# Kernel optimization log

Hardware: AMD Instinct MI355X
Metric: run time of the kernel (lower is better)

Reference implementation:

```python
import jax, jax.numpy as jnp
import numpy as np

NUM_EDGE = 5
NUM_CHANNELS = 2
NUM_NODES = 2048
W_IN = 256
W_OUT = 128
NUM_CLASS = 16
NUM_LAYERS = 2


def gtconv(A, w):
    """Softmax-weighted mix of edge-type adjacencies.
    A: [E, N, N], w: [E, C] -> [C, N, N].
    Equivalent to concatenating COO edge lists scaled by filter[j, i] and
    summing duplicates (what the scipy round-trip does implicitly)."""
    f = jax.nn.softmax(w, axis=0)  # softmax over edge types (dim=0)
    return jnp.einsum('enm,ec->cnm', A, f)


def degree_normalize(H):
    """GTN.normalization: deg = scatter_add over col, value *= deg[col]^-1 (col scaling).
    H: [C, N, N]; deg over rows (axis=1) gives per-column in-degree."""
    deg = H.sum(axis=1)  # [C, N]
    dinv = jnp.where(deg > 0, 1.0 / jnp.where(deg > 0, deg, 1.0), 0.0)
    return H * dinv[:, None, :]


def setup_inputs() -> dict:
    key = jax.random.key(0)
    ks = jax.random.split(key, 8)
    A = jax.random.uniform(ks[0], (NUM_EDGE, NUM_NODES, NUM_NODES), dtype=jnp.float32)
    h = jax.random.normal(ks[1], (NUM_NODES, W_IN), dtype=jnp.float32)
    # GTConv weights: init std=0.01 as in reset_parameters
    w1 = jax.random.normal(ks[2], (NUM_EDGE, NUM_CHANNELS), dtype=jnp.float32) * 0.01
    w2 = jax.random.normal(ks[3], (NUM_EDGE, NUM_CHANNELS), dtype=jnp.float32) * 0.01
    w_layers = jax.random.normal(ks[4], (NUM_LAYERS - 1, NUM_EDGE, NUM_CHANNELS), dtype=jnp.float32) * 0.01
    gcn_w = jax.random.normal(ks[5], (W_IN, W_OUT), dtype=jnp.float32) * (1.0 / np.sqrt(W_IN))
    gcn_b = jnp.zeros((W_OUT,), dtype=jnp.float32)
    lin1_w = jax.random.normal(ks[6], (W_OUT * NUM_CHANNELS, W_OUT), dtype=jnp.float32) * (1.0 / np.sqrt(W_OUT * NUM_CHANNELS))
    lin1_b = jnp.zeros((W_OUT,), dtype=jnp.float32)
    lin2_w = jax.random.normal(ks[7], (W_OUT, NUM_CLASS), dtype=jnp.float32) * (1.0 / np.sqrt(W_OUT))
    lin2_b = jnp.zeros((NUM_CLASS,), dtype=jnp.float32)
    return {"A": A, "h": h, "w1": w1, "w2": w2, "w_layers": w_layers,
            "gcn_w": gcn_w, "gcn_b": gcn_b, "lin1_w": lin1_w, "lin1_b": lin1_b,
            "lin2_w": lin2_w, "lin2_b": lin2_b}


def reference(A, h, w1, w2, w_layers, gcn_w, gcn_b, lin1_w, lin1_b, lin2_w, lin2_b):
    # Layer 0 (first=True): H[c] = conv1(A)[c] @ conv2(A)[c], then degree norm.
    H = jnp.einsum('cnk,ckm->cnm', gtconv(A, w1), gtconv(A, w2))
    H = degree_normalize(H)
    # Layers 1..L-1 (first=False): H[c] = H[c] @ conv(A)[c], then degree norm.
    for i in range(w_layers.shape[0]):
        B = gtconv(A, w_layers[i])
        H = jnp.einsum('cnk,ckm->cnm', H, B)
        H = degree_normalize(H)
    # Shared GCN per channel (DGL GraphConv, norm='both'): weight first (w_in > w_out),
    # src out-degree^-1/2 scaling, aggregate along edges src->dst, dst in-degree^-1/2.
    hw = h @ gcn_w                                   # [N, w_out]
    dout = jnp.clip(H.sum(axis=2), 1.0, None) ** -0.5  # [C, N] src norm
    din = jnp.clip(H.sum(axis=1), 1.0, None) ** -0.5   # [C, N] dst norm
    agg = jnp.einsum('cnm,cnd->cmd', H, dout[:, :, None] * hw[None])  # dst m gathers from src n
    X = jax.nn.relu(agg * din[:, :, None] + gcn_b)   # [C, N, w_out]
    # Concatenate channels along feature dim (channel-major, matching th.cat order)
    X = jnp.transpose(X, (1, 0, 2)).reshape(H.shape[1], -1)  # [N, C*w_out]
    X = jax.nn.relu(X @ lin1_w + lin1_b)
    return X @ lin2_w + lin2_b
```

## Files before the change

### kernel.cpp

```cpp
#include <hip/hip_runtime.h>

typedef unsigned short u16;
typedef __attribute__((ext_vector_type(4))) float f32x4;
typedef __attribute__((ext_vector_type(8))) __bf16 bf16x8;
typedef __attribute__((ext_vector_type(8))) unsigned short us8;

#define NN (2048ull*2048ull)

__device__ __forceinline__ u16 f2b(float x){
  union { float f; unsigned u; } v; v.f = x;
  unsigned r = v.u + 0x7FFFu + ((v.u >> 16) & 1u);
  return (u16)(r >> 16);
}
__device__ __forceinline__ float b2f(u16 x){
  union { unsigned u; float f; } v; v.u = ((unsigned)x) << 16; return v.f;
}

__global__ __launch_bounds__(256)
void k_mix(const float* __restrict__ A,
           const float* __restrict__ w1, const float* __restrict__ w2,
           const float* __restrict__ wl,
           u16* __restrict__ A1, u16* __restrict__ A2T, u16* __restrict__ BT,
           float* __restrict__ zbuf){
  __shared__ u16 lt[4][64][72];
  const int t = threadIdx.x;
  if (blockIdx.x == 0 && blockIdx.y == 0){
    #pragma unroll
    for (int i=0;i<48;i++) zbuf[i*256 + t] = 0.f;
  }
  const int mq = t & 15, nr = t >> 4;
  const int n0 = blockIdx.y * 64, m0 = blockIdx.x * 64;
  float f[3][2][5];
  #pragma unroll
  for (int s=0;s<3;s++){
    const float* w = (s==0) ? w1 : (s==1) ? w2 : wl;
    #pragma unroll
    for (int c=0;c<2;c++){
      float m = -1e30f;
      #pragma unroll
      for (int e=0;e<5;e++) m = fmaxf(m, w[e*2+c]);
      float sum = 0.f;
      #pragma unroll
      for (int e=0;e<5;e++){ f[s][c][e] = __expf(w[e*2+c]-m); sum += f[s][c][e]; }
      float inv = 1.f/sum;
      #pragma unroll
      for (int e=0;e<5;e++) f[s][c][e] *= inv;
    }
  }

  #pragma unroll
  for (int rr=0; rr<4; ++rr){
    const int nl = nr*4 + rr;
    const size_t off = (size_t)(n0+nl)*2048 + m0 + mq*4;
    float4 a0 = *(const float4*)&A[off];
    float4 a1 = *(const float4*)&A[NN + off];
    float4 a2 = *(const float4*)&A[2*NN + off];
    float4 a3 = *(const float4*)&A[3*NN + off];
    float4 a4 = *(const float4*)&A[4*NN + off];
    float ax[4][5] = {{a0.x,a1.x,a2.x,a3.x,a4.x},
                      {a0.y,a1.y,a2.y,a3.y,a4.y},
                      {a0.z,a1.z,a2.z,a3.z,a4.z},
                      {a0.w,a1.w,a2.w,a3.w,a4.w}};
    #pragma unroll
    for (int c=0;c<2;c++){
      ushort4 o1, o2, o3;
      #pragma unroll
      for (int j=0;j<4;j++){
        float s1=0.f,s2=0.f,s3=0.f;
        #pragma unroll
        for (int e=0;e<5;e++){
          s1 += ax[j][e]*f[0][c][e];
          s2 += ax[j][e]*f[1][c][e];
          s3 += ax[j][e]*f[2][c][e];
        }
        ((u16*)&o1)[j] = f2b(s1);
        ((u16*)&o2)[j] = f2b(s2);
        ((u16*)&o3)[j] = f2b(s3);
      }
      *(ushort4*)&A1[(size_t)c*NN + off] = o1;
      *(ushort4*)&lt[c][nl][mq*4] = o2;
      *(ushort4*)&lt[2+c][nl][mq*4] = o3;
    }
  }
  __syncthreads();
  const int nq = t & 15, mr = t >> 4;
  #pragma unroll
  for (int s=0;s<4;s++){
    u16* __restrict__ dst = (s<2) ? A2T : BT;
    const int c = s & 1;
    #pragma unroll
    for (int rr=0;rr<4;rr++){
      const int ml = mr*4 + rr;
      ushort4 o;
      o.x = lt[s][nq*4+0][ml];
      o.y = lt[s][nq*4+1][ml];
      o.z = lt[s][nq*4+2][ml];
      o.w = lt[s][nq*4+3][ml];
      *(ushort4*)&dst[(size_t)c*NN + (size_t)(m0+ml)*2048 + n0 + nq*4] = o;
    }
  }
}

template<bool TRANS>
__global__ __launch_bounds__(512, 2)
void k_gemm_big(const u16* __restrict__ A, const u16* __restrict__ Bt,
                u16* __restrict__ C, float* __restrict__ deg){
  __shared__ u16 lA[2][256*64];
  __shared__ u16 lB[2][128*64];
  const int tid = threadIdx.x;
  const int bm = blockIdx.x, bn = blockIdx.y, cc = blockIdx.z;
  const u16* __restrict__ Ab = A + (size_t)cc*NN + (size_t)(bm*256)*2048;
  const u16* __restrict__ Bb = Bt + (size_t)cc*NN + (size_t)(bn*128)*2048;
  const int wid = tid >> 6, lane = tid & 63;
  const int wr = wid >> 1, wc = wid & 1;
  const int fl = lane & 15, fkg = lane >> 4;
  const int srow = tid >> 3;
  const int scol_sw = ((tid & 7) ^ (srow & 7)) << 3;
  const int csw0 = (((0*4 + fkg) ^ (fl & 7)) << 3);
  const int csw1 = (((1*4 + fkg) ^ (fl & 7)) << 3);

  f32x4 acc[4][4];
  const f32x4 zero = {0.f,0.f,0.f,0.f};
  #pragma unroll
  for (int i=0;i<4;i++)
    #pragma unroll
    for (int jj=0;jj<4;jj++) acc[i][jj] = zero;

  auto stage = [&](int buf, int k0){
    #pragma unroll
    for (int i=0;i<4;++i)
      __builtin_amdgcn_global_load_lds(
        (const __attribute__((address_space(1))) void*)(Ab + (size_t)(i*64 + srow)*2048 + k0 + scol_sw),
        (__attribute__((address_space(3))) void*)(&lA[buf][(i*512 + (wid<<6))<<3]), 16, 0, 0);
    #pragma unroll
    for (int i=0;i<2;++i)
      __builtin_amdgcn_global_load_lds(
        (const __attribute__((address_space(1))) void*)(Bb + (size_t)(i*64 + srow)*2048 + k0 + scol_sw),
        (__attribute__((address_space(3))) void*)(&lB[buf][(i*512 + (wid<<6))<<3]), 16, 0, 0);
  };

  auto compute = [&](const u16* __restrict__ ca, const u16* __restrict__ cb){
    bf16x8 af[2][4], bfr[2][4];
    #pragma unroll
    for (int mi=0;mi<4;mi++){
      af[0][mi] = *reinterpret_cast<const bf16x8*>(&ca[(wr*64 + mi*16 + fl)*64 + csw0]);
      af[1][mi] = *reinterpret_cast<const bf16x8*>(&ca[(wr*64 + mi*16 + fl)*64 + csw1]);
    }
    #pragma unroll
    for (int ni=0;ni<4;ni++){
      bfr[0][ni] = *reinterpret_cast<const bf16x8*>(&cb[(wc*64 + ni*16 + fl)*64 + csw0]);
      bfr[1][ni] = *reinterpret_cast<const bf16x8*>(&cb[(wc*64 + ni*16 + fl)*64 + csw1]);
    }
    __builtin_amdgcn_sched_barrier(0);
    __builtin_amdgcn_s_setprio(1);
    #pragma unroll
    for (int ks=0; ks<2; ++ks)
      #pragma unroll
      for (int mi=0;mi<4;mi++)
        #pragma unroll
        for (int ni=0;ni<4;ni++)
          acc[mi][ni] = __builtin_amdgcn_mfma_f32_16x16x32_bf16(af[ks][mi], bfr[ks][ni], acc[mi][ni], 0, 0, 0);
    __builtin_amdgcn_s_setprio(0);
    __builtin_amdgcn_sched_barrier(0);
  };

  stage(0, 0);
  stage(1, 64);
  int cur = 0;
  #pragma unroll 2
  for (int t = 0; t < 30; ++t){
    asm volatile("s_waitcnt vmcnt(6)" ::: "memory");
    __builtin_amdgcn_sched_barrier(0);
    __builtin_amdgcn_s_barrier();
    __builtin_amdgcn_sched_barrier(0);
    compute(&lA[cur][0], &lB[cur][0]);
    __builtin_amdgcn_s_barrier();
    __builtin_amdgcn_sched_barrier(0);
    stage(cur, (t+2)*64);
    cur ^= 1;
  }
  asm volatile("s_waitcnt vmcnt(6)" ::: "memory");
  __builtin_amdgcn_sched_barrier(0);
  __builtin_amdgcn_s_barrier();
  __builtin_amdgcn_sched_barrier(0);
  compute(&lA[cur][0], &lB[cur][0]);
  cur ^= 1;
  asm volatile("s_waitcnt vmcnt(0)" ::: "memory");
  __builtin_amdgcn_sched_barrier(0);
  __builtin_amdgcn_s_barrier();
  __builtin_amdgcn_sched_barrier(0);
  compute(&lA[cur][0], &lB[cur][0]);

  #pragma unroll
  for (int ni=0; ni<4; ++ni){
    float cs = 0.f;
    #pragma unroll
    for (int mi=0;mi<4;mi++)
      #pragma unroll
      for (int r=0;r<4;r++) cs += acc[mi][ni][r];
    cs += __shfl_xor(cs, 16);
    cs += __shfl_xor(cs, 32);
    if (lane < 16)
      atomicAdd(&deg[cc*2048 + bn*128 + wc*64 + ni*16 + fl], cs);
  }
  const int rbase = fkg << 2;
  if (!TRANS){
    u16* __restrict__ Cb = C + (size_t)cc*NN + (size_t)(bm*256 + wr*64)*2048 + bn*128 + wc*64;
    #pragma unroll
    for (int mi=0;mi<4;mi++)
      #pragma unroll
      for (int ni=0;ni<4;ni++)
        #pragma unroll
        for (int r=0;r<4;r++)
          Cb[(size_t)(mi*16 + rbase + r)*2048 + ni*16 + fl] = f2b(acc[mi][ni][r]);
  } else {
    u16* __restrict__ Cb = C + (size_t)cc*NN + (size_t)(bn*128 + wc*64)*2048 + bm*256 + wr*64;
    #pragma unroll
    for (int ni=0;ni<4;ni++)
      #pragma unroll
      for (int mi=0;mi<4;mi++){
        ushort4 o;
        o.x = f2b(acc[mi][ni][0]); o.y = f2b(acc[mi][ni][1]);
        o.z = f2b(acc[mi][ni][2]); o.w = f2b(acc[mi][ni][3]);
        *(ushort4*)&Cb[(size_t)(ni*16 + fl)*2048 + mi*16 + rbase] = o;
      }
  }
}

__global__ void k_btscale(u16* __restrict__ BT, const float* __restrict__ deg){
  size_t idx = (size_t)blockIdx.x*256 + threadIdx.x;
  int c  = (int)(idx >> 19);
  int k8 = ((int)(idx & 255)) * 8;
  us8 v = ((const us8*)BT)[idx];
  #pragma unroll
  for (int j=0;j<8;j++){
    float d = deg[c*2048 + k8 + j];
    float di = d > 0.f ? 1.f/d : 0.f;
    v[j] = f2b(b2f(v[j]) * di);
  }
  ((us8*)BT)[idx] = v;
}

__global__ __launch_bounds__(256)
void k_wcolsum(const u16* __restrict__ HT, const float* __restrict__ deg2,
               float* __restrict__ rowsum){
  __shared__ float sdi[128];
  const int t = threadIdx.x;
  const int n = blockIdx.x * 256 + t;
  const int m0 = blockIdx.y * 128;
  const int c = blockIdx.z;
  if (t < 128){
    float d = deg2[c*2048 + m0 + t];
    sdi[t] = d > 0.f ? 1.f/d : 0.f;
  }
  __syncthreads();
  const u16* __restrict__ p = HT + (size_t)c*NN + (size_t)m0*2048 + n;
  float s = 0.f;
  #pragma unroll 4
  for (int m=0;m<128;m++)
    s += b2f(p[(size_t)m*2048]) * sdi[m];
  atomicAdd(&rowsum[c*2048 + n], s);
}

__global__ __launch_bounds__(256)
void k_hw(const float* __restrict__ h, const float* __restrict__ W, float* __restrict__ hw){
  __shared__ float lh[16][256];
  int t = threadIdx.x;
  int n0 = blockIdx.x * 16;
  for (int idx = t; idx < 16*256; idx += 256)
    lh[idx >> 8][idx & 255] = h[(size_t)(n0 + (idx>>8))*256 + (idx&255)];
  __syncthreads();
  int d = t & 127, half = t >> 7;
  float acc[8];
  #pragma unroll
  for (int nn=0;nn<8;nn++) acc[nn] = 0.f;
  for (int k=0;k<256;k++){
    float wv = W[(size_t)k*128 + d];
    #pragma unroll
    for (int nn=0;nn<8;nn++) acc[nn] += lh[half*8+nn][k]*wv;
  }
  #pragma unroll
  for (int nn=0;nn<8;nn++) hw[(size_t)(n0 + half*8 + nn)*128 + d] = acc[nn];
}

__global__ void k_pt(const float* __restrict__ hw, const float* __restrict__ rowsum,
                     u16* __restrict__ PT){
  int t = threadIdx.x;
  int n = blockIdx.x * 64 + (t & 63);
  int c = blockIdx.y;
  float dv = rsqrtf(fmaxf(rowsum[c*2048 + n], 1.0f));
  for (int d = t >> 6; d < 128; d += 4)
    PT[((size_t)c*128 + d)*2048 + n] = f2b(dv * hw[(size_t)n*128 + d]);
}

__global__ __launch_bounds__(256, 2)
void k_gemm3(const u16* __restrict__ A, const u16* __restrict__ Bt, float* __restrict__ Cp){
  __shared__ u16 lA[128*64];
  __shared__ u16 lB[128*64];
  const int tid = threadIdx.x;
  const int bm = blockIdx.x, bk = blockIdx.y, cc = blockIdx.z;
  const u16* __restrict__ Ab = A + (size_t)cc*NN + (size_t)(bm*128)*2048 + bk*256;
  const u16* __restrict__ Bb = Bt + (size_t)cc*(128*2048) + bk*256;
  float* __restrict__ Cb = Cp + ((size_t)bk*2 + cc)*2048*128 + (size_t)(bm*128)*128;
  const int wid = tid >> 6, lane = tid & 63;
  const int wr = wid >> 1, wc = wid & 1;
  const int fl = lane & 15, fk = (lane >> 4) << 3;
  const int srow = (wid << 3) + (lane >> 3);
  const int scol = (lane & 7) << 3;

  f32x4 acc[4][4];
  const f32x4 zero = {0.f,0.f,0.f,0.f};
  #pragma unroll
  for (int i=0;i<4;i++)
    #pragma unroll
    for (int jj=0;jj<4;jj++) acc[i][jj] = zero;

  for (int k0 = 0; k0 < 256; k0 += 64){
    #pragma unroll
    for (int it = 0; it < 4; ++it){
      int r = it*32 + srow;
      __builtin_amdgcn_global_load_lds(
        (const __attribute__((address_space(1))) void*)(Ab + (size_t)r*2048 + k0 + scol),
        (__attribute__((address_space(3))) void*)(&lA[(it*32 + (wid<<3))*64]), 16, 0, 0);
      __builtin_amdgcn_global_load_lds(
        (const __attribute__((address_space(1))) void*)(Bb + (size_t)r*2048 + k0 + scol),
        (__attribute__((address_space(3))) void*)(&lB[(it*32 + (wid<<3))*64]), 16, 0, 0);
    }
    __syncthreads();
    #pragma unroll
    for (int ks = 0; ks < 2; ++ks){
      bf16x8 af[4], bfr[4];
      #pragma unroll
      for (int mi=0;mi<4;mi++)
        af[mi] = *reinterpret_cast<const bf16x8*>(&lA[(wr*64 + mi*16 + fl)*64 + ks*32 + fk]);
      #pragma unroll
      for (int ni=0;ni<4;ni++)
        bfr[ni] = *reinterpret_cast<const bf16x8*>(&lB[(wc*64 + ni*16 + fl)*64 + ks*32 + fk]);
      #pragma unroll
      for (int mi=0;mi<4;mi++)
        #pragma unroll
        for (int ni=0;ni<4;ni++)
          acc[mi][ni] = __builtin_amdgcn_mfma_f32_16x16x32_bf16(af[mi], bfr[ni], acc[mi][ni], 0, 0, 0);
    }
    __syncthreads();
  }
  const int rbase = (lane >> 4) << 2;
  #pragma unroll
  for (int mi=0;mi<4;mi++)
    #pragma unroll
    for (int ni=0;ni<4;ni++)
      #pragma unroll
      for (int r=0;r<4;r++)
        Cb[(size_t)(wr*64 + mi*16 + rbase + r)*128 + wc*64 + ni*16 + fl] = acc[mi][ni][r];
}

__global__ __launch_bounds__(256)
void k_head(const float* __restrict__ aggp, const float* __restrict__ deg2,
            const float* __restrict__ gb,
            const float* __restrict__ W1, const float* __restrict__ b1,
            const float* __restrict__ W2, const float* __restrict__ b2,
            float* __restrict__ out){
  __shared__ float lx[16][256];
  __shared__ float lt[16][132];
  int t = threadIdx.x;
  int n0 = blockIdx.x * 16;
  for (int idx = t; idx < 1024; idx += 256){
    int row = idx >> 6;
    int q = idx & 63;
    int c = q >> 5, d4 = (q & 31) * 4;
    float dg = deg2[c*2048 + n0 + row];
    float di = dg > 0.f ? 1.f/dg : 0.f;
    float4 s = {0.f,0.f,0.f,0.f};
    #pragma unroll
    for (int p=0;p<8;p++){
      const float4 v = *(const float4*)&aggp[(((size_t)p*2 + c)*2048 + n0 + row)*128 + d4];
      s.x += v.x; s.y += v.y; s.z += v.z; s.w += v.w;
    }
    const float4 bv = *(const float4*)&gb[d4];
    s.x = fmaxf(s.x*di + bv.x, 0.f); s.y = fmaxf(s.y*di + bv.y, 0.f);
    s.z = fmaxf(s.z*di + bv.z, 0.f); s.w = fmaxf(s.w*di + bv.w, 0.f);
    *(float4*)&lx[row][c*128 + d4] = s;
  }
  __syncthreads();
  int d = t & 127, half = t >> 7;
  float acc[8];
  #pragma unroll
  for (int nn=0;nn<8;nn++) acc[nn] = 0.f;
  for (int k=0;k<256;k++){
    float wv = W1[(size_t)k*128 + d];
    #pragma unroll
    for (int nn=0;nn<8;nn++) acc[nn] += lx[half*8+nn][k]*wv;
  }
  float bb = b1[d];
  #pragma unroll
  for (int nn=0;nn<8;nn++){
    float v = acc[nn] + bb;
    lt[half*8+nn][d] = v > 0.f ? v : 0.f;
  }
  __syncthreads();
  {
    int row = t >> 4, q = t & 15;
    float s = b2[q];
    for (int dd=0; dd<128; dd++) s += lt[row][dd] * W2[(size_t)dd*16 + q];
    out[(size_t)(n0+row)*16 + q] = s;
  }
}

extern "C" void kernel_launch(void* const* d_in, const int* in_sizes, int n_in,
                              void* d_out, int out_size, void* d_ws, size_t ws_size,
                              hipStream_t stream){
  const float* A   = (const float*)d_in[0];
  const float* h   = (const float*)d_in[1];
  const float* w1  = (const float*)d_in[2];
  const float* w2  = (const float*)d_in[3];
  const float* wl  = (const float*)d_in[4];
  const float* gw  = (const float*)d_in[5];
  const float* gb  = (const float*)d_in[6];
  const float* l1w = (const float*)d_in[7];
  const float* l1b = (const float*)d_in[8];
  const float* l2w = (const float*)d_in[9];
  const float* l2b = (const float*)d_in[10];
  float* out = (float*)d_out;
  char* ws = (char*)d_ws;

  const size_t SZ = 2*NN*2;
  u16*  A1   = (u16*)(ws);
  u16*  A2T  = (u16*)(ws + 1*SZ);
  u16*  BT   = (u16*)(ws + 2*SZ);
  u16*  Hbf  = (u16*)(ws + 3*SZ);
  u16*  HT   = (u16*)(ws + 4*SZ);
  float* aggp= (float*)(ws + 5*SZ);
  char* tail = ws + 6*SZ;
  float* hw    = (float*)tail;
  u16*  PT     = (u16*)(tail + 2048*128*4);
  float* deg1  = (float*)(tail + 2048*128*4 + 2*128*2048*2);
  float* deg2  = deg1 + 4096;
  float* rowsum= deg2 + 4096;

  const size_t TOTAL = 6*SZ + 2048*128*4 + (size_t)2*128*2048*2 + 3*4096*4;
  if (ws_size < TOTAL){ hipMemsetAsync(d_out, 0, (size_t)out_size*4, stream); return; }

  k_mix<<<dim3(32,32), 256, 0, stream>>>(A, w1, w2, wl, A1, A2T, BT, deg1);
  k_gemm_big<false><<<dim3(8,16,2), 512, 0, stream>>>(A1, A2T, Hbf, deg1);
  k_btscale<<<4096, 256, 0, stream>>>(BT, deg1);
  k_gemm_big<true><<<dim3(8,16,2), 512, 0, stream>>>(Hbf, BT, HT, deg2);
  k_wcolsum<<<dim3(8,16,2), 256, 0, stream>>>(HT, deg2, rowsum);
  k_hw<<<128, 256, 0, stream>>>(h, gw, hw);
  k_pt<<<dim3(32,2), 256, 0, stream>>>(hw, rowsum, PT);
  k_gemm3<<<dim3(16,8,2), 256, 0, stream>>>(HT, PT, aggp);
  k_head<<<128, 256, 0, stream>>>(aggp, deg2, gb, l1w, l1b, l2w, l2b, out);
}
```

Measured before the change: 174.5 us.

## Use 4-wave GEMM blocks with 128x64 warp tiles and triple-buffered LDS

Result: slower. 198.6 us (+13.8%).

```diff
diff --git a/kernel.cpp b/kernel.cpp
--- a/kernel.cpp
+++ b/kernel.cpp
@@ -102,11 +102,11 @@
 }
 
 template<bool TRANS>
-__global__ __launch_bounds__(512, 2)
+__global__ __launch_bounds__(256, 1)
 void k_gemm_big(const u16* __restrict__ A, const u16* __restrict__ Bt,
                 u16* __restrict__ C, float* __restrict__ deg){
-  __shared__ u16 lA[2][256*64];
-  __shared__ u16 lB[2][128*64];
+  __shared__ u16 lA[3][256*64];
+  __shared__ u16 lB[3][128*64];
   const int tid = threadIdx.x;
   const int bm = blockIdx.x, bn = blockIdx.y, cc = blockIdx.z;
   const u16* __restrict__ Ab = A + (size_t)cc*NN + (size_t)(bm*256)*2048;
@@ -116,75 +116,77 @@
   const int fl = lane & 15, fkg = lane >> 4;
   const int srow = tid >> 3;
   const int scol_sw = ((tid & 7) ^ (srow & 7)) << 3;
-  const int csw0 = (((0*4 + fkg) ^ (fl & 7)) << 3);
-  const int csw1 = (((1*4 + fkg) ^ (fl & 7)) << 3);
-
-  f32x4 acc[4][4];
+
+  f32x4 acc[8][4];
   const f32x4 zero = {0.f,0.f,0.f,0.f};
   #pragma unroll
-  for (int i=0;i<4;i++)
+  for (int i=0;i<8;i++)
     #pragma unroll
     for (int jj=0;jj<4;jj++) acc[i][jj] = zero;
 
   auto stage = [&](int buf, int k0){
+    #pragma unroll
+    for (int i=0;i<8;++i)
+      __builtin_amdgcn_global_load_lds(
+        (const __attribute__((address_space(1))) void*)(Ab + (size_t)(i*32 + srow)*2048 + k0 + scol_sw),
+        (__attribute__((address_space(3))) void*)(&lA[buf][(i*32 + (wid<<3))*64]), 16, 0, 0);
     #pragma unroll
     for (int i=0;i<4;++i)
       __builtin_amdgcn_global_load_lds(
-        (const __attribute__((address_space(1))) void*)(Ab + (size_t)(i*64 + srow)*2048 + k0 + scol_sw),
-        (__attribute__((address_space(3))) void*)(&lA[buf][(i*512 + (wid<<6))<<3]), 16, 0, 0);
-    #pragma unroll
-    for (int i=0;i<2;++i)
-      __builtin_amdgcn_global_load_lds(
-        (const __attribute__((address_space(1))) void*)(Bb + (size_t)(i*64 + srow)*2048 + k0 + scol_sw),
-        (__attribute__((address_space(3))) void*)(&lB[buf][(i*512 + (wid<<6))<<3]), 16, 0, 0);
+        (const __attribute__((address_space(1))) void*)(Bb + (size_t)(i*32 + srow)*2048 + k0 + scol_sw),
+        (__attribute__((address_space(3))) void*)(&lB[buf][(i*32 + (wid<<3))*64]), 16, 0, 0);
   };
 
   auto compute = [&](const u16* __restrict__ ca, const u16* __restrict__ cb){
-    bf16x8 af[2][4], bfr[2][4];
-    #pragma unroll
-    for (int mi=0;mi<4;mi++){
-      af[0][mi] = *reinterpret_cast<const bf16x8*>(&ca[(wr*64 + mi*16 + fl)*64 + csw0]);
-      af[1][mi] = *reinterpret_cast<const bf16x8*>(&ca[(wr*64 + mi*16 + fl)*64 + csw1]);
-    }
-    #pragma unroll
-    for (int ni=0;ni<4;ni++){
-      bfr[0][ni] = *reinterpret_cast<const bf16x8*>(&cb[(wc*64 + ni*16 + fl)*64 + csw0]);
-      bfr[1][ni] = *reinterpret_cast<const bf16x8*>(&cb[(wc*64 + ni*16 + fl)*64 + csw1]);
-    }
-    __builtin_amdgcn_sched_barrier(0);
-    __builtin_amdgcn_s_setprio(1);
-    #pragma unroll
-    for (int ks=0; ks<2; ++ks)
-      #pragma unroll
-      for (int mi=0;mi<4;mi++)
+    #pragma unroll
+    for (int ks=0; ks<2; ++ks){
+      const int csw = (((ks*4 + fkg) ^ (fl & 7)) << 3);
+      bf16x8 af[8], bfr[4];
+      #pragma unroll
+      for (int mi=0;mi<8;mi++)
+        af[mi] = *reinterpret_cast<const bf16x8*>(&ca[(wr*128 + mi*16 + fl)*64 + csw]);
+      #pragma unroll
+      for (int ni=0;ni<4;ni++)
+        bfr[ni] = *reinterpret_cast<const bf16x8*>(&cb[(wc*64 + ni*16 + fl)*64 + csw]);
+      __builtin_amdgcn_sched_barrier(0);
+      __builtin_amdgcn_s_setprio(1);
+      #pragma unroll
+      for (int mi=0;mi<8;mi++)
         #pragma unroll
         for (int ni=0;ni<4;ni++)
-          acc[mi][ni] = __builtin_amdgcn_mfma_f32_16x16x32_bf16(af[ks][mi], bfr[ks][ni], acc[mi][ni], 0, 0, 0);
-    __builtin_amdgcn_s_setprio(0);
-    __builtin_amdgcn_sched_barrier(0);
+          acc[mi][ni] = __builtin_amdgcn_mfma_f32_16x16x32_bf16(af[mi], bfr[ni], acc[mi][ni], 0, 0, 0);
+      __builtin_amdgcn_s_setprio(0);
+      __builtin_amdgcn_sched_barrier(0);
+    }
   };
 
   stage(0, 0);
   stage(1, 64);
+  stage(2, 128);
   int cur = 0;
-  #pragma unroll 2
-  for (int t = 0; t < 30; ++t){
-    asm volatile("s_waitcnt vmcnt(6)" ::: "memory");
+  for (int t = 0; t < 29; ++t){
+    asm volatile("s_waitcnt vmcnt(24)" ::: "memory");
     __builtin_amdgcn_sched_barrier(0);
     __builtin_amdgcn_s_barrier();
     __builtin_amdgcn_sched_barrier(0);
     compute(&lA[cur][0], &lB[cur][0]);
     __builtin_amdgcn_s_barrier();
     __builtin_amdgcn_sched_barrier(0);
-    stage(cur, (t+2)*64);
-    cur ^= 1;
-  }
-  asm volatile("s_waitcnt vmcnt(6)" ::: "memory");
+    stage(cur, (t+3)*64);
+    cur = (cur == 2) ? 0 : cur + 1;
+  }
+  asm volatile("s_waitcnt vmcnt(24)" ::: "memory");
   __builtin_amdgcn_sched_barrier(0);
   __builtin_amdgcn_s_barrier();
   __builtin_amdgcn_sched_barrier(0);
   compute(&lA[cur][0], &lB[cur][0]);
-  cur ^= 1;
+  cur = (cur == 2) ? 0 : cur + 1;
+  asm volatile("s_waitcnt vmcnt(12)" ::: "memory");
+  __builtin_amdgcn_sched_barrier(0);
+  __builtin_amdgcn_s_barrier();
+  __builtin_amdgcn_sched_barrier(0);
+  compute(&lA[cur][0], &lB[cur][0]);
+  cur = (cur == 2) ? 0 : cur + 1;
   asm volatile("s_waitcnt vmcnt(0)" ::: "memory");
   __builtin_amdgcn_sched_barrier(0);
   __builtin_amdgcn_s_barrier();
@@ -195,7 +197,7 @@
   for (int ni=0; ni<4; ++ni){
     float cs = 0.f;
     #pragma unroll
-    for (int mi=0;mi<4;mi++)
+    for (int mi=0;mi<8;mi++)
       #pragma unroll
       for (int r=0;r<4;r++) cs += acc[mi][ni][r];
     cs += __shfl_xor(cs, 16);
@@ -205,20 +207,20 @@
   }
   const int rbase = fkg << 2;
   if (!TRANS){
-    u16* __restrict__ Cb = C + (size_t)cc*NN + (size_t)(bm*256 + wr*64)*2048 + bn*128 + wc*64;
-    #pragma unroll
-    for (int mi=0;mi<4;mi++)
+    u16* __restrict__ Cb = C + (size_t)cc*NN + (size_t)(bm*256 + wr*128)*2048 + bn*128 + wc*64;
+    #pragma unroll
+    for (int mi=0;mi<8;mi++)
       #pragma unroll
       for (int ni=0;ni<4;ni++)
         #pragma unroll
         for (int r=0;r<4;r++)
           Cb[(size_t)(mi*16 + rbase + r)*2048 + ni*16 + fl] = f2b(acc[mi][ni][r]);
   } else {
-    u16* __restrict__ Cb = C + (size_t)cc*NN + (size_t)(bn*128 + wc*64)*2048 + bm*256 + wr*64;
+    u16* __restrict__ Cb = C + (size_t)cc*NN + (size_t)(bn*128 + wc*64)*2048 + bm*256 + wr*128;
     #pragma unroll
     for (int ni=0;ni<4;ni++)
       #pragma unroll
-      for (int mi=0;mi<4;mi++){
+      for (int mi=0;mi<8;mi++){
         ushort4 o;
         o.x = f2b(acc[mi][ni][0]); o.y = f2b(acc[mi][ni][1]);
         o.z = f2b(acc[mi][ni][2]); o.w = f2b(acc[mi][ni][3]);
@@ -441,9 +443,9 @@
   if (ws_size < TOTAL){ hipMemsetAsync(d_out, 0, (size_t)out_size*4, stream); return; }
 
   k_mix<<<dim3(32,32), 256, 0, stream>>>(A, w1, w2, wl, A1, A2T, BT, deg1);
-  k_gemm_big<false><<<dim3(8,16,2), 512, 0, stream>>>(A1, A2T, Hbf, deg1);
+  k_gemm_big<false><<<dim3(8,16,2), 256, 0, stream>>>(A1, A2T, Hbf, deg1);
   k_btscale<<<4096, 256, 0, stream>>>(BT, deg1);
-  k_gemm_big<true><<<dim3(8,16,2), 512, 0, stream>>>(Hbf, BT, HT, deg2);
+  k_gemm_big<true><<<dim3(8,16,2), 256, 0, stream>>>(Hbf, BT, HT, deg2);
   k_wcolsum<<<dim3(8,16,2), 256, 0, stream>>>(HT, deg2, rowsum);
   k_hw<<<128, 256, 0, stream>>>(h, gw, hw);
   k_pt<<<dim3(32,2), 256, 0, stream>>>(hw, rowsum, PT);
```
